# Kernel tuning notes

Measured on AMD Instinct MI355X. Metric: run time of the kernel, lower is better.

Reference implementation:

```python
import jax, jax.numpy as jnp
import numpy as np

N_POINTS = 500_000
D_PHASE = 6
N_BINS = 128
LO, HI = -4.0, 4.0


def setup_inputs() -> dict:
    key = jax.random.key(0)
    x = jax.random.normal(key, (N_POINTS, D_PHASE), dtype=jnp.float32)
    edges_x = jnp.linspace(LO, HI, N_BINS + 1, dtype=jnp.float32)
    edges_y = jnp.linspace(LO, HI, N_BINS + 1, dtype=jnp.float32)
    return {"x": x, "edges_x": edges_x, "edges_y": edges_y}


def reference(x, edges_x, edges_y):
    # Histogram2D(axis=(0,1), bandwidth=(1.0,1.0), kde=True).forward(x)
    # bin centers from edges
    cx = 0.5 * (edges_x[:-1] + edges_x[1:])  # (nx,)
    cy = 0.5 * (edges_y[:-1] + edges_y[1:])  # (ny,)
    # resolution = first bin width; bandwidth = 1.0 * resolution
    bwx = edges_x[1] - edges_x[0]
    bwy = edges_y[1] - edges_y[0]
    # per-point Gaussian kernel evaluations against bin centers
    kx = jnp.exp(-0.5 * jnp.square((x[:, 0][:, None] - cx[None, :]) / bwx))  # (n, nx)
    ky = jnp.exp(-0.5 * jnp.square((x[:, 1][:, None] - cy[None, :]) / bwy))  # (n, ny)
    # accumulate joint KDE histogram via outer-product contraction over points
    hist = jnp.einsum("ni,nj->ij", kx, ky)  # (nx, ny)
    # normalize to a probability density (integrates to 1 over the grid)
    hist = hist / (jnp.sum(hist) * bwx * bwy)
    return hist
```

## Files before the change

### kernel.cpp

```cpp
#include <hip/hip_runtime.h>

#define NBINS 128
#define NB2   (NBINS * NBINS)
#define TPB   1024
#define NBLK  256
#define KC    64
#define NTEAM 4

typedef __attribute__((ext_vector_type(8)))  short short8;
typedef __attribute__((ext_vector_type(16))) float f32x16;

__device__ __forceinline__ float exp2_fast(float x) {
#if defined(__has_builtin)
#if __has_builtin(__builtin_amdgcn_exp2f)
    return __builtin_amdgcn_exp2f(x);
#else
    return exp2f(x);
#endif
#else
    return exp2f(x);
#endif
}

__device__ __forceinline__ unsigned pk_bf16(float a, float b) {
    const unsigned ar = __float_as_uint(a) + 0x8000u;
    const unsigned br = __float_as_uint(b) + 0x8000u;
    return __builtin_amdgcn_perm(br, ar, 0x07060302u);
}

#define WC (-0.72134752044448170f)

union S8 { short8 s; unsigned u[4]; };

__global__ __launch_bounds__(TPB, 4) void kde_mfma_kernel(
    const float* __restrict__ x,
    const float* __restrict__ ex,
    const float* __restrict__ ey,
    float* __restrict__ out,
    int n, int nchunks)
{
    __shared__ float hist[NB2];
    __shared__ __align__(16) float u_s[2][NTEAM][KC];
    __shared__ __align__(16) float v_s[2][NTEAM][KC];

    const int tid  = (int)threadIdx.x;
    const int lane = tid & 63;
    const int half = lane >> 5;
    const int l31  = lane & 31;
    const int w4   = (tid >> 6) & 3;
    const int team = tid >> 8;
    const int rowblk = (w4 >> 1) * 64;
    const int colblk = (w4 & 1) * 64;
    const float rowf = (float)(rowblk + l31);
    const float colf = (float)(colblk + l31);

    const float lox = ex[0], loy = ey[0];
    const float ibx = 1.0f / (ex[1] - ex[0]);
    const float iby = 1.0f / (ey[1] - ey[0]);

    f32x16 acc[2][2];
    #pragma unroll
    for (int a = 0; a < 2; ++a)
        #pragma unroll
        for (int c = 0; c < 2; ++c)
            #pragma unroll
            for (int r = 0; r < 16; ++r) acc[a][c][r] = 0.f;

    auto stage = [&](int it, int bb) {
        if (tid < NTEAM * KC) {
            const int tm  = tid >> 6, idx = tid & 63;
            const int g   = (int)blockIdx.x * NTEAM + tm + it * (NBLK * NTEAM);
            if (g < nchunks) {
                const int p = g * KC + idx;
                float uu = 1e9f, vv = 1e9f;
                if (p < n) {
                    const float2 xy = *(const float2*)(x + (size_t)p * 6);
                    uu = (xy.x - lox) * ibx - 0.5f;
                    vv = (xy.y - loy) * iby - 0.5f;
                }
                u_s[bb][tm][idx] = uu; v_s[bb][tm][idx] = vv;
            }
        }
    };

    const int niter = (nchunks + NBLK * NTEAM - 1) / (NBLK * NTEAM);
    stage(0, 0);
    for (int it = 0; it < niter; ++it) {
        __syncthreads();
        if (it + 1 < niter) stage(it + 1, (it + 1) & 1);
        const int bb = it & 1;
        const int g = (int)blockIdx.x * NTEAM + team + it * (NBLK * NTEAM);
        if (g < nchunks) {
            const float* us = u_s[bb][team];
            const float* vs = v_s[bb][team];
            #pragma unroll
            for (int s4 = 0; s4 < 4; ++s4) {
                const int kb = s4 * 16 + half * 8;
                const float4 ua = *(const float4*)&us[kb];
                const float4 ub = *(const float4*)&us[kb + 4];
                const float4 va = *(const float4*)&vs[kb];
                const float4 vb = *(const float4*)&vs[kb + 4];

                S8 af[2], bf[2];
                #pragma unroll
                for (int rb = 0; rb < 2; ++rb) {
                    const float m = rowf + (float)(rb * 32);
                    float d0 = ua.x - m, d1 = ua.y - m, d2 = ua.z - m, d3 = ua.w - m;
                    float d4 = ub.x - m, d5 = ub.y - m, d6 = ub.z - m, d7 = ub.w - m;
                    const float w0 = exp2_fast((WC * d0) * d0);
                    const float w1 = exp2_fast((WC * d1) * d1);
                    const float w2 = exp2_fast((WC * d2) * d2);
                    const float w3 = exp2_fast((WC * d3) * d3);
                    const float w4f = exp2_fast((WC * d4) * d4);
                    const float w5 = exp2_fast((WC * d5) * d5);
                    const float w6 = exp2_fast((WC * d6) * d6);
                    const float w7 = exp2_fast((WC * d7) * d7);
                    af[rb].u[0] = pk_bf16(w0, w1);
                    af[rb].u[1] = pk_bf16(w2, w3);
                    af[rb].u[2] = pk_bf16(w4f, w5);
                    af[rb].u[3] = pk_bf16(w6, w7);
                }
                #pragma unroll
                for (int tj = 0; tj < 2; ++tj) {
                    const float c = colf + (float)(tj * 32);
                    float d0 = va.x - c, d1 = va.y - c, d2 = va.z - c, d3 = va.w - c;
                    float d4 = vb.x - c, d5 = vb.y - c, d6 = vb.z - c, d7 = vb.w - c;
                    const float w0 = exp2_fast((WC * d0) * d0);
                    const float w1 = exp2_fast((WC * d1) * d1);
                    const float w2 = exp2_fast((WC * d2) * d2);
                    const float w3 = exp2_fast((WC * d3) * d3);
                    const float w4f = exp2_fast((WC * d4) * d4);
                    const float w5 = exp2_fast((WC * d5) * d5);
                    const float w6 = exp2_fast((WC * d6) * d6);
                    const float w7 = exp2_fast((WC * d7) * d7);
                    bf[tj].u[0] = pk_bf16(w0, w1);
                    bf[tj].u[1] = pk_bf16(w2, w3);
                    bf[tj].u[2] = pk_bf16(w4f, w5);
                    bf[tj].u[3] = pk_bf16(w6, w7);
                }
                #pragma unroll
                for (int rb = 0; rb < 2; ++rb)
                    #pragma unroll
                    for (int tj = 0; tj < 2; ++tj)
                        acc[rb][tj] = __builtin_amdgcn_mfma_f32_32x32x16_bf16(
                            af[rb].s, bf[tj].s, acc[rb][tj], 0, 0, 0);
            }
        }
    }
    __syncthreads();

    for (int tm = 0; tm < NTEAM; ++tm) {
        if (team == tm) {
            #pragma unroll
            for (int rb = 0; rb < 2; ++rb)
                #pragma unroll
                for (int tj = 0; tj < 2; ++tj)
                    #pragma unroll
                    for (int r = 0; r < 16; ++r) {
                        const int row = rowblk + rb * 32 + (r & 3) + 8 * (r >> 2) + 4 * half;
                        const int col = colblk + tj * 32 + l31;
                        const int a = row * NBINS + col;
                        const float v = acc[rb][tj][r];
                        if (tm == 0) hist[a] = v;
                        else         hist[a] += v;
                    }
        }
        __syncthreads();
    }

    for (int i = tid; i < NB2; i += TPB)
        unsafeAtomicAdd(&out[i], hist[i]);
}

__global__ __launch_bounds__(TPB) void kde_final_kernel(
    float* __restrict__ out,
    const float* __restrict__ ex,
    const float* __restrict__ ey)
{
    __shared__ float red[TPB / 64];
    __shared__ float sinv;
    const int tid = (int)threadIdx.x;

    float4 v[4];
    float s = 0.f;
    #pragma unroll
    for (int i = 0; i < 4; ++i) {
        v[i] = ((const float4*)out)[tid + i * TPB];
        s += v[i].x + v[i].y + v[i].z + v[i].w;
    }
    #pragma unroll
    for (int off = 32; off > 0; off >>= 1) s += __shfl_down(s, off, 64);
    if ((tid & 63) == 0) red[tid >> 6] = s;
    __syncthreads();
    if (tid == 0) {
        float t = 0.f;
        #pragma unroll
        for (int i = 0; i < TPB / 64; ++i) t += red[i];
        sinv = 1.0f / (t * (ex[1] - ex[0]) * (ey[1] - ey[0]));
    }
    __syncthreads();
    const float inv = sinv;
    #pragma unroll
    for (int i = 0; i < 4; ++i) {
        float4 o = v[i];
        o.x *= inv; o.y *= inv; o.z *= inv; o.w *= inv;
        ((float4*)out)[tid + i * TPB] = o;
    }
}

extern "C" void kernel_launch(void* const* d_in, const int* in_sizes, int n_in,
                              void* d_out, int out_size, void* d_ws, size_t ws_size,
                              hipStream_t stream)
{
    const float* x  = (const float*)d_in[0];
    const float* ex = (const float*)d_in[1];
    const float* ey = (const float*)d_in[2];
    float* out = (float*)d_out;
    const int n = in_sizes[0] / 6;
    const int nchunks = (n + KC - 1) / KC;

    hipMemsetAsync(d_out, 0, NB2 * sizeof(float), stream);
    kde_mfma_kernel<<<NBLK, TPB, 0, stream>>>(x, ex, ey, out, n, nchunks);
    kde_final_kernel<<<1, TPB, 0, stream>>>(out, ex, ey);
}
```

Measured before the change: 126.1 us.

## Generate Gaussian weights by recurrence into shared-memory tiles, pipelined with MFMA

Before, each lane computed one exp2 per bin-point pair for every MFMA operand. Now each thread evaluates a few exp2 at the window centre and fills 16 bins around it using the multiplicative Gaussian recurrence (ratio updated by e^-1). The bf16 tiles are written to swizzled shared memory, and MFMA reads them back, with weight generation for the next chunk overlapped with MFMA on the current one via double buffering. This cuts transcendental work sharply but adds shared-memory traffic and a larger LDS footprint (union with hist), and the recurrence may lose accuracy over 8 steps.

After: 110.7 us. 12.2% less time.

```diff
diff --git a/kernel.cpp b/kernel.cpp
--- a/kernel.cpp
+++ b/kernel.cpp
@@ -4,8 +4,9 @@
 #define NB2   (NBINS * NBINS)
 #define TPB   1024
 #define NBLK  256
-#define KC    64
+#define KC    32
 #define NTEAM 4
+#define ROWB  (KC * 2)
 
 typedef __attribute__((ext_vector_type(8)))  short short8;
 typedef __attribute__((ext_vector_type(16))) float f32x16;
@@ -29,8 +30,15 @@
 }
 
 #define WC (-0.72134752044448170f)
-
-union S8 { short8 s; unsigned u[4]; };
+#define E1 (0.36787944117144233f)
+
+union __align__(16) ShMem {
+    struct {
+        unsigned short tiles[2][NTEAM][2][NBINS][KC];
+        float uv[2][NTEAM][2][KC];
+    } s;
+    float hist[NB2];
+};
 
 __global__ __launch_bounds__(TPB, 4) void kde_mfma_kernel(
     const float* __restrict__ x,
@@ -39,9 +47,7 @@
     float* __restrict__ out,
     int n, int nchunks)
 {
-    __shared__ float hist[NB2];
-    __shared__ __align__(16) float u_s[2][NTEAM][KC];
-    __shared__ __align__(16) float v_s[2][NTEAM][KC];
+    __shared__ ShMem sm;
 
     const int tid  = (int)threadIdx.x;
     const int lane = tid & 63;
@@ -51,13 +57,17 @@
     const int team = tid >> 8;
     const int rowblk = (w4 >> 1) * 64;
     const int colblk = (w4 & 1) * 64;
-    const float rowf = (float)(rowblk + l31);
-    const float colf = (float)(colblk + l31);
 
     const float lox = ex[0], loy = ey[0];
     const float ibx = 1.0f / (ex[1] - ex[0]);
     const float iby = 1.0f / (ey[1] - ey[0]);
 
+    const int tt     = tid & 255;
+    const int pI     = tt & 15;
+    const int dimi   = (tt >> 4) & 1;
+    const int eighth = tt >> 5;
+    const float cc   = (float)(eighth * 16 + 8);
+
     f32x16 acc[2][2];
     #pragma unroll
     for (int a = 0; a < 2; ++a)
@@ -66,10 +76,12 @@
             #pragma unroll
             for (int r = 0; r < 16; ++r) acc[a][c][r] = 0.f;
 
-    auto stage = [&](int it, int bb) {
-        if (tid < NTEAM * KC) {
-            const int tm  = tid >> 6, idx = tid & 63;
-            const int g   = (int)blockIdx.x * NTEAM + tm + it * (NBLK * NTEAM);
+    const int niter = (nchunks + NBLK * NTEAM - 1) / (NBLK * NTEAM);
+
+    auto stage = [&](int jt) {
+        if (tid < NTEAM * KC && jt < niter) {
+            const int tm = tid >> 5, idx = tid & 31;
+            const int g  = (int)blockIdx.x * NTEAM + tm + jt * (NBLK * NTEAM);
             if (g < nchunks) {
                 const int p = g * KC + idx;
                 float uu = 1e9f, vv = 1e9f;
@@ -78,76 +90,79 @@
                     uu = (xy.x - lox) * ibx - 0.5f;
                     vv = (xy.y - loy) * iby - 0.5f;
                 }
-                u_s[bb][tm][idx] = uu; v_s[bb][tm][idx] = vv;
+                sm.s.uv[jt & 1][tm][0][idx] = uu;
+                sm.s.uv[jt & 1][tm][1][idx] = vv;
             }
         }
     };
 
-    const int niter = (nchunks + NBLK * NTEAM - 1) / (NBLK * NTEAM);
-    stage(0, 0);
+    auto gen = [&](int jt) {
+        const int g = (int)blockIdx.x * NTEAM + team + jt * (NBLK * NTEAM);
+        if (g >= nchunks) return;
+        const int bb = jt & 1;
+        const float* uvp = sm.s.uv[bb][team][dimi];
+        const float u0 = uvp[2 * pI], u1 = uvp[2 * pI + 1];
+        const float d0 = fminf(fmaxf(u0 - cc, -88.f), 88.f);
+        const float d1 = fminf(fmaxf(u1 - cc, -88.f), 88.f);
+        const float w0 = exp2_fast((WC * d0) * d0);
+        const float w1 = exp2_fast((WC * d1) * d1);
+        float r0 = exp2_fast(fmaf(-2.f * WC, d0, WC));
+        float r1 = exp2_fast(fmaf(-2.f * WC, d1, WC));
+        float q0 = exp2_fast(fmaf( 2.f * WC, d0, WC));
+        float q1 = exp2_fast(fmaf( 2.f * WC, d1, WC));
+        char* tb0 = (char*)&sm.s.tiles[bb][team][dimi][0][0]
+                  + (eighth * 16 + 8) * ROWB;
+        const int o0 = pI << 2;
+        const int os[4] = { o0, o0 ^ 16, o0 ^ 32, o0 ^ 48 };
+        float a0 = w0, a1 = w1;
+        #pragma unroll
+        for (int j = 0; j < 8; ++j) {
+            *(unsigned*)(tb0 + j * ROWB + os[j & 3]) = pk_bf16(a0, a1);
+            a0 *= r0; r0 *= E1;
+            a1 *= r1; r1 *= E1;
+        }
+        a0 = w0; a1 = w1;
+        #pragma unroll
+        for (int j = 1; j <= 8; ++j) {
+            a0 *= q0; a1 *= q1;
+            *(unsigned*)(tb0 - j * ROWB + os[(4 - j) & 3]) = pk_bf16(a0, a1);
+            q0 *= E1; q1 *= E1;
+        }
+    };
+
+    auto domfma = [&](int it) {
+        const int g = (int)blockIdx.x * NTEAM + team + it * (NBLK * NTEAM);
+        if (g >= nchunks) return;
+        const int bb = it & 1;
+        const char* Ab = (const char*)&sm.s.tiles[bb][team][0][0][0];
+        const char* Bb = (const char*)&sm.s.tiles[bb][team][1][0][0];
+        const int ra = rowblk + l31, ca = colblk + l31;
+        const int swa = (ra & 3) << 4, swb = (ca & 3) << 4;
+        #pragma unroll
+        for (int s4 = 0; s4 < 2; ++s4) {
+            const int kb2 = s4 * 32 + half * 16;
+            const short8 a0 = *(const short8*)(Ab + ra * ROWB        + (kb2 ^ swa));
+            const short8 a1 = *(const short8*)(Ab + (ra + 32) * ROWB + (kb2 ^ swa));
+            const short8 b0 = *(const short8*)(Bb + ca * ROWB        + (kb2 ^ swb));
+            const short8 b1 = *(const short8*)(Bb + (ca + 32) * ROWB + (kb2 ^ swb));
+            acc[0][0] = __builtin_amdgcn_mfma_f32_32x32x16_bf16(a0, b0, acc[0][0], 0, 0, 0);
+            acc[0][1] = __builtin_amdgcn_mfma_f32_32x32x16_bf16(a0, b1, acc[0][1], 0, 0, 0);
+            acc[1][0] = __builtin_amdgcn_mfma_f32_32x32x16_bf16(a1, b0, acc[1][0], 0, 0, 0);
+            acc[1][1] = __builtin_amdgcn_mfma_f32_32x32x16_bf16(a1, b1, acc[1][1], 0, 0, 0);
+        }
+    };
+
+    stage(0);
+    __syncthreads();
+    stage(1);
+    gen(0);
+    __syncthreads();
     for (int it = 0; it < niter; ++it) {
+        stage(it + 2);
+        domfma(it);
+        gen(it + 1);
         __syncthreads();
-        if (it + 1 < niter) stage(it + 1, (it + 1) & 1);
-        const int bb = it & 1;
-        const int g = (int)blockIdx.x * NTEAM + team + it * (NBLK * NTEAM);
-        if (g < nchunks) {
-            const float* us = u_s[bb][team];
-            const float* vs = v_s[bb][team];
-            #pragma unroll
-            for (int s4 = 0; s4 < 4; ++s4) {
-                const int kb = s4 * 16 + half * 8;
-                const float4 ua = *(const float4*)&us[kb];
-                const float4 ub = *(const float4*)&us[kb + 4];
-                const float4 va = *(const float4*)&vs[kb];
-                const float4 vb = *(const float4*)&vs[kb + 4];
-
-                S8 af[2], bf[2];
-                #pragma unroll
-                for (int rb = 0; rb < 2; ++rb) {
-                    const float m = rowf + (float)(rb * 32);
-                    float d0 = ua.x - m, d1 = ua.y - m, d2 = ua.z - m, d3 = ua.w - m;
-                    float d4 = ub.x - m, d5 = ub.y - m, d6 = ub.z - m, d7 = ub.w - m;
-                    const float w0 = exp2_fast((WC * d0) * d0);
-                    const float w1 = exp2_fast((WC * d1) * d1);
-                    const float w2 = exp2_fast((WC * d2) * d2);
-                    const float w3 = exp2_fast((WC * d3) * d3);
-                    const float w4f = exp2_fast((WC * d4) * d4);
-                    const float w5 = exp2_fast((WC * d5) * d5);
-                    const float w6 = exp2_fast((WC * d6) * d6);
-                    const float w7 = exp2_fast((WC * d7) * d7);
-                    af[rb].u[0] = pk_bf16(w0, w1);
-                    af[rb].u[1] = pk_bf16(w2, w3);
-                    af[rb].u[2] = pk_bf16(w4f, w5);
-                    af[rb].u[3] = pk_bf16(w6, w7);
-                }
-                #pragma unroll
-                for (int tj = 0; tj < 2; ++tj) {
-                    const float c = colf + (float)(tj * 32);
-                    float d0 = va.x - c, d1 = va.y - c, d2 = va.z - c, d3 = va.w - c;
-                    float d4 = vb.x - c, d5 = vb.y - c, d6 = vb.z - c, d7 = vb.w - c;
-                    const float w0 = exp2_fast((WC * d0) * d0);
-                    const float w1 = exp2_fast((WC * d1) * d1);
-                    const float w2 = exp2_fast((WC * d2) * d2);
-                    const float w3 = exp2_fast((WC * d3) * d3);
-                    const float w4f = exp2_fast((WC * d4) * d4);
-                    const float w5 = exp2_fast((WC * d5) * d5);
-                    const float w6 = exp2_fast((WC * d6) * d6);
-                    const float w7 = exp2_fast((WC * d7) * d7);
-                    bf[tj].u[0] = pk_bf16(w0, w1);
-                    bf[tj].u[1] = pk_bf16(w2, w3);
-                    bf[tj].u[2] = pk_bf16(w4f, w5);
-                    bf[tj].u[3] = pk_bf16(w6, w7);
-                }
-                #pragma unroll
-                for (int rb = 0; rb < 2; ++rb)
-                    #pragma unroll
-                    for (int tj = 0; tj < 2; ++tj)
-                        acc[rb][tj] = __builtin_amdgcn_mfma_f32_32x32x16_bf16(
-                            af[rb].s, bf[tj].s, acc[rb][tj], 0, 0, 0);
-            }
-        }
-    }
-    __syncthreads();
+    }
 
     for (int tm = 0; tm < NTEAM; ++tm) {
         if (team == tm) {
@@ -161,15 +176,15 @@
                         const int col = colblk + tj * 32 + l31;
                         const int a = row * NBINS + col;
                         const float v = acc[rb][tj][r];
-                        if (tm == 0) hist[a] = v;
-                        else         hist[a] += v;
+                        if (tm == 0) sm.hist[a] = v;
+                        else         sm.hist[a] += v;
                     }
         }
         __syncthreads();
     }
 
     for (int i = tid; i < NB2; i += TPB)
-        unsafeAtomicAdd(&out[i], hist[i]);
+        unsafeAtomicAdd(&out[i], sm.hist[i]);
 }
 
 __global__ __launch_bounds__(TPB) void kde_final_kernel(
```
